# Kernel tuning notes

Hardware: AMD Instinct MI355X
Metric: run time of the kernel (lower is better)

Reference implementation:

```python
import math
import jax, jax.numpy as jnp
import numpy as np

B, S, D, H, DFF, MEM = 4, 1024, 1024, 16, 4096, 256
HD = D // H  # 64
EPS = 1e-5


def _ln(x, g, b):
    mu = jnp.mean(x, axis=-1, keepdims=True)
    var = jnp.mean(jnp.square(x - mu), axis=-1, keepdims=True)
    return (x - mu) * jax.lax.rsqrt(var + EPS) * g + b


def _rope(x, cos, sin):
    # x: (b, h, s, hd); cos/sin: (>=s, hd//2)
    s = x.shape[2]
    xp = x.reshape(*x.shape[:-1], -1, 2)
    x0, x1 = xp[..., 0], xp[..., 1]
    c = cos[:s][None, None]
    sn = sin[:s][None, None]
    r0 = x0 * c - x1 * sn
    r1 = x0 * sn + x1 * c
    return jnp.stack([r0, r1], axis=-1).reshape(x.shape)


def setup_inputs() -> dict:
    key = jax.random.key(0)
    ks = jax.random.split(key, 16)
    p = lambda k, shape: jax.random.normal(k, shape, dtype=jnp.float32) * 0.02

    tgt = jax.random.normal(ks[0], (B, S, D), dtype=jnp.float32)
    memory = jax.random.normal(ks[1], (B, MEM, D), dtype=jnp.float32)

    # causal additive mask (s, s)
    tgt_mask = jnp.where(jnp.tril(jnp.ones((S, S), bool)), 0.0, -1e9).astype(jnp.float32)

    # RoPE freqs, theta=10000
    inv_freq = 1.0 / (10000.0 ** (np.arange(0, HD, 2, dtype=np.float32) / HD))
    ang = np.arange(S, dtype=np.float32)[:, None] * inv_freq[None, :]
    rope_cos = jnp.asarray(np.cos(ang))
    rope_sin = jnp.asarray(np.sin(ang))

    return {
        "tgt": tgt, "memory": memory, "tgt_mask": tgt_mask,
        "rope_cos": rope_cos, "rope_sin": rope_sin,
        "qkv_w": p(ks[2], (3 * D, D)), "qkv_b": jnp.zeros((3 * D,), jnp.float32),
        "out_w": p(ks[3], (D, D)), "out_b": jnp.zeros((D,), jnp.float32),
        "ca_in_w": p(ks[4], (3 * D, D)), "ca_in_b": jnp.zeros((3 * D,), jnp.float32),
        "ca_out_w": p(ks[5], (D, D)), "ca_out_b": jnp.zeros((D,), jnp.float32),
        "ffn_w1": p(ks[6], (DFF, D)), "ffn_b1": jnp.zeros((DFF,), jnp.float32),
        "ffn_w2": p(ks[7], (D, DFF)), "ffn_b2": jnp.zeros((D,), jnp.float32),
        "ln1_g": jnp.ones((D,), jnp.float32), "ln1_b": jnp.zeros((D,), jnp.float32),
        "ln2_g": jnp.ones((D,), jnp.float32), "ln2_b": jnp.zeros((D,), jnp.float32),
        "ln3_g": jnp.ones((D,), jnp.float32), "ln3_b": jnp.zeros((D,), jnp.float32),
    }


def reference(tgt, memory, tgt_mask, rope_cos, rope_sin,
              qkv_w, qkv_b, out_w, out_b,
              ca_in_w, ca_in_b, ca_out_w, ca_out_b,
              ffn_w1, ffn_b1, ffn_w2, ffn_b2,
              ln1_g, ln1_b, ln2_g, ln2_b, ln3_g, ln3_b):
    b, s, d = tgt.shape
    scale = 1.0 / math.sqrt(HD)

    # ---- self-attention with RoPE ----
    x = _ln(tgt, ln1_g, ln1_b)
    qkv = (x @ qkv_w.T + qkv_b).reshape(b, s, 3, H, HD)
    qkv = jnp.transpose(qkv, (2, 0, 3, 1, 4))  # (3, b, h, s, hd)
    q, k, v = qkv[0], qkv[1], qkv[2]
    q = _rope(q, rope_cos, rope_sin)
    k = _rope(k, rope_cos, rope_sin)
    attn = jnp.einsum('bhqd,bhkd->bhqk', q, k) * scale
    attn = attn + tgt_mask[None, None]
    attn = jax.nn.softmax(attn, axis=-1)
    sa = jnp.einsum('bhqk,bhkd->bhqd', attn, v)
    sa = jnp.transpose(sa, (0, 2, 1, 3)).reshape(b, s, d)
    tgt = tgt + (sa @ out_w.T + out_b)

    # ---- cross-attention (standard MHA, no positional encoding) ----
    x = _ln(tgt, ln2_g, ln2_b)
    wq, wk, wv = jnp.split(ca_in_w, 3, axis=0)
    bq, bk, bv = jnp.split(ca_in_b, 3, axis=0)
    m = memory.shape[1]
    cq = (x @ wq.T + bq).reshape(b, s, H, HD).transpose(0, 2, 1, 3)
    ck = (memory @ wk.T + bk).reshape(b, m, H, HD).transpose(0, 2, 1, 3)
    cv = (memory @ wv.T + bv).reshape(b, m, H, HD).transpose(0, 2, 1, 3)
    cattn = jax.nn.softmax(jnp.einsum('bhqd,bhkd->bhqk', cq, ck) * scale, axis=-1)
    co = jnp.einsum('bhqk,bhkd->bhqd', cattn, cv)
    co = jnp.transpose(co, (0, 2, 1, 3)).reshape(b, s, d)
    tgt = tgt + (co @ ca_out_w.T + ca_out_b)

    # ---- FFN (exact GELU, as torch nn.GELU default) ----
    x = _ln(tgt, ln3_g, ln3_b)
    ff = jax.nn.gelu(x @ ffn_w1.T + ffn_b1, approximate=False) @ ffn_w2.T + ffn_b2
    return tgt + ff
```

## Files before the change

kernel.cpp:

```cpp
#include <hip/hip_runtime.h>
#include <hip/hip_bf16.h>


using bf16 = __hip_bfloat16;
typedef __bf16 bf16x8 __attribute__((ext_vector_type(8)));
typedef float f32x4 __attribute__((ext_vector_type(4)));

static constexpr int Bn = 4, Ssz = 1024, Dm = 1024, Hh = 16, HDd = 64, DFFn = 4096, MEMn = 256;

__device__ inline float bf2f(bf16 x) { return __bfloat162float(x); }
__device__ inline bf16 f2bf(float x) { return __float2bfloat16(x); }

__device__ __forceinline__ void gload16(const bf16* g, bf16* l) {
  __builtin_amdgcn_global_load_lds(
      (const __attribute__((address_space(1))) void*)g,
      (__attribute__((address_space(3))) void*)l, 16, 0, 0);
}

__global__ void detect_kernel(const unsigned* __restrict__ cosw, int* __restrict__ flag) {
  if (threadIdx.x == 0) *flag = (cosw[0] == 0x3F800000u) ? 1 : 0;
}

struct CanonArgs {
  const void* src[23];
  void* dst[23];
  int n[23];
};
__global__ __launch_bounds__(256) void canon_all(CanonArgs a, float* __restrict__ resid,
                                                 const int* __restrict__ flagp) {
  const int seg = blockIdx.y;
  const int n4 = a.n[seg] >> 2;
  if (n4 == 0) return;
  const int fl = *flagp;
  if (fl) {
    const float4* s = (const float4*)a.src[seg];
    bf16* d = (bf16*)a.dst[seg];
    for (int i = blockIdx.x * 256 + threadIdx.x; i < n4; i += gridDim.x * 256) {
      float4 v = s[i];
      bf16 t[4] = {f2bf(v.x), f2bf(v.y), f2bf(v.z), f2bf(v.w)};
      *reinterpret_cast<unsigned long long*>(d + i * 4) =
          *reinterpret_cast<unsigned long long*>(t);
      if (seg == 0) *reinterpret_cast<float4*>(resid + i * 4) = v;
    }
  } else {
    const unsigned long long* s = (const unsigned long long*)a.src[seg];
    unsigned long long* d = (unsigned long long*)a.dst[seg];
    for (int i = blockIdx.x * 256 + threadIdx.x; i < n4; i += gridDim.x * 256) {
      unsigned long long v = s[i];
      d[i] = v;
      if (seg == 0) {
        const unsigned short* u = reinterpret_cast<const unsigned short*>(&v);
        float4 f;
        f.x = __uint_as_float(((unsigned)u[0]) << 16);
        f.y = __uint_as_float(((unsigned)u[1]) << 16);
        f.z = __uint_as_float(((unsigned)u[2]) << 16);
        f.w = __uint_as_float(((unsigned)u[3]) << 16);
        *reinterpret_cast<float4*>(resid + i * 4) = f;
      }
    }
  }
}

__global__ __launch_bounds__(256) void ln_kernel(const float* __restrict__ x,
                                                 const bf16* __restrict__ g,
                                                 const bf16* __restrict__ bb,
                                                 bf16* __restrict__ y) {
  const int row = blockIdx.x;
  const float* xr = x + (size_t)row * Dm;
  const int i0 = threadIdx.x * 4;
  float4 v = *reinterpret_cast<const float4*>(xr + i0);
  float s = v.x + v.y + v.z + v.w;
  float ss = v.x * v.x + v.y * v.y + v.z * v.z + v.w * v.w;
#pragma unroll
  for (int o = 32; o > 0; o >>= 1) {
    s += __shfl_down(s, o);
    ss += __shfl_down(ss, o);
  }
  __shared__ float shs[4], shss[4];
  const int wave = threadIdx.x >> 6, lane = threadIdx.x & 63;
  if (lane == 0) { shs[wave] = s; shss[wave] = ss; }
  __syncthreads();
  s = shs[0] + shs[1] + shs[2] + shs[3];
  ss = shss[0] + shss[1] + shss[2] + shss[3];
  const float mu = s * (1.0f / Dm);
  const float var = fmaxf(ss * (1.0f / Dm) - mu * mu, 0.0f);
  const float rs = rsqrtf(var + 1e-5f);
  bf16* yr = y + (size_t)row * Dm + i0;
  float vv[4] = {v.x, v.y, v.z, v.w};
#pragma unroll
  for (int j = 0; j < 4; ++j)
    yr[j] = f2bf((vv[j] - mu) * rs * bf2f(g[i0 + j]) + bf2f(bb[i0 + j]));
}

__global__ __launch_bounds__(256) void gemm_bt(
    const bf16* __restrict__ A, const bf16* __restrict__ W,
    const bf16* __restrict__ bias, bf16* __restrict__ outB, float* __restrict__ outF,
    const float* __restrict__ residIn, float* __restrict__ residOut,
    const int* __restrict__ flagp, int M, int N, int K, int epi) {
  __shared__ bf16 As[64][40];
  __shared__ bf16 Ws[64][40];
  const int tid = threadIdx.x;
  const int m0 = blockIdx.x * 64, n0 = blockIdx.y * 64;
  const int wave = tid >> 6, lane = tid & 63;
  const int wm = wave >> 1, wn = wave & 1;
  const int quad = lane >> 4, m16 = lane & 15;
  const int lr = tid >> 2, lc = (tid & 3) * 8;

  f32x4 acc[2][2] = {};

  const bf16* Ap = A + (size_t)(m0 + lr) * K + lc;
  const bf16* Wp = W + (size_t)(n0 + lr) * K + lc;
  for (int k0 = 0; k0 < K; k0 += 32) {
    float4 av = *reinterpret_cast<const float4*>(Ap + k0);
    float4 wv = *reinterpret_cast<const float4*>(Wp + k0);
    *reinterpret_cast<float4*>(&As[lr][lc]) = av;
    *reinterpret_cast<float4*>(&Ws[lr][lc]) = wv;
    __syncthreads();
    bf16x8 aF[2], bF[2];
#pragma unroll
    for (int t = 0; t < 2; ++t) {
      aF[t] = *reinterpret_cast<const bf16x8*>(&As[wm * 32 + t * 16 + m16][quad * 8]);
      bF[t] = *reinterpret_cast<const bf16x8*>(&Ws[wn * 32 + t * 16 + m16][quad * 8]);
    }
#pragma unroll
    for (int mt = 0; mt < 2; ++mt)
#pragma unroll
      for (int nt = 0; nt < 2; ++nt)
        acc[mt][nt] = __builtin_amdgcn_mfma_f32_16x16x32_bf16(aF[mt], bF[nt], acc[mt][nt], 0, 0, 0);
    __syncthreads();
  }
  const int fl = (epi == 3) ? *flagp : 0;
#pragma unroll
  for (int mt = 0; mt < 2; ++mt) {
#pragma unroll
    for (int nt = 0; nt < 2; ++nt) {
      const int col = n0 + wn * 32 + nt * 16 + m16;
      const float bv = bf2f(bias[col]);
#pragma unroll
      for (int r = 0; r < 4; ++r) {
        const int row = m0 + wm * 32 + mt * 16 + quad * 4 + r;
        const size_t idx = (size_t)row * N + col;
        float v = acc[mt][nt][r] + bv;
        if (epi == 0) {
          outB[idx] = f2bf(v);
        } else if (epi == 1) {
          outB[idx] = f2bf(0.5f * v * (1.0f + erff(v * 0.70710678118654752f)));
        } else if (epi == 2) {
          residOut[idx] = residIn[idx] + v;
        } else {
          const float rr = residIn[idx] + v;
          if (fl) outF[idx] = rr; else outB[idx] = f2bf(rr);
        }
      }
    }
  }
}

__global__ __launch_bounds__(512) void gemm128(
    const bf16* __restrict__ A, const bf16* __restrict__ W,
    const bf16* __restrict__ bias, bf16* __restrict__ outB, float* __restrict__ outF,
    const float* __restrict__ residIn, float* __restrict__ residOut,
    const int* __restrict__ flagp, int M, int N, int K, int epi) {
  __shared__ bf16 As[4][128][32];
  __shared__ bf16 Ws[4][128][32];
  const int tid = threadIdx.x;
  const int wave = tid >> 6, lane = tid & 63;
  const int wm = wave >> 1;
  const int wn = wave & 1;
  const int quad = lane >> 4, m16 = lane & 15;
  const int m0 = blockIdx.x * 128, n0 = blockIdx.y * 128;

  const int sr = tid >> 2;
  const int sc = (tid & 3) * 8;
  const bf16* Ap = A + (size_t)(m0 + sr) * K + sc;
  const bf16* Wp = W + (size_t)(n0 + sr) * K + sc;

  f32x4 acc[2][4] = {};

#define STAGE128(T, BUF)                                   \
  {                                                        \
    const int kk_ = (T) * 32;                              \
    gload16(Ap + kk_, &As[BUF][sr][sc]);                   \
    gload16(Wp + kk_, &Ws[BUF][sr][sc]);                   \
  }

#define READS128(RB)                                                                        \
  _Pragma("unroll") for (int tt = 0; tt < 2; ++tt)                                          \
    aF[tt] = *reinterpret_cast<const bf16x8*>(&As[RB][wm * 32 + tt * 16 + m16][quad * 8]);  \
  _Pragma("unroll") for (int nt = 0; nt < 4; ++nt)                                          \
    bF[nt] = *reinterpret_cast<const bf16x8*>(&Ws[RB][wn * 64 + nt * 16 + m16][quad * 8]);

#define MFMAS128                                                                            \
  _Pragma("unroll") for (int mt = 0; mt < 2; ++mt)                                          \
  _Pragma("unroll") for (int nt = 0; nt < 4; ++nt)                                          \
    acc[mt][nt] = __builtin_amdgcn_mfma_f32_16x16x32_bf16(aF[mt], bF[nt], acc[mt][nt], 0, 0, 0);

  const int nsteps = K >> 5;
  STAGE128(0, 0)
  STAGE128(1, 1)
  STAGE128(2, 2)

  int rb = 0, sb = 3;
  for (int t = 0; t < nsteps - 2; ++t) {
    asm volatile("s_waitcnt vmcnt(4)" ::: "memory");
    __builtin_amdgcn_s_barrier();
    __builtin_amdgcn_sched_barrier(0);
    bf16x8 aF[2], bF[4];
    READS128(rb)
    __builtin_amdgcn_sched_barrier(0);
    if (t + 3 < nsteps) { STAGE128(t + 3, sb) }
    __builtin_amdgcn_sched_barrier(0);
    MFMAS128
    rb = (rb + 1 == 4) ? 0 : rb + 1;
    sb = (sb + 1 == 4) ? 0 : sb + 1;
  }
  {
    asm volatile("s_waitcnt vmcnt(2)" ::: "memory");
    __builtin_amdgcn_s_barrier();
    __builtin_amdgcn_sched_barrier(0);
    bf16x8 aF[2], bF[4];
    READS128(rb)
    MFMAS128
    rb = (rb + 1 == 4) ? 0 : rb + 1;
  }
  {
    asm volatile("s_waitcnt vmcnt(0)" ::: "memory");
    __builtin_amdgcn_s_barrier();
    __builtin_amdgcn_sched_barrier(0);
    bf16x8 aF[2], bF[4];
    READS128(rb)
    MFMAS128
  }
#undef STAGE128
#undef READS128
#undef MFMAS128

  const int fl = (epi == 3) ? *flagp : 0;
#pragma unroll
  for (int mt = 0; mt < 2; ++mt) {
#pragma unroll
    for (int nt = 0; nt < 4; ++nt) {
      const int col = n0 + wn * 64 + nt * 16 + m16;
      const float bv = bf2f(bias[col]);
#pragma unroll
      for (int r = 0; r < 4; ++r) {
        const int row = m0 + wm * 32 + mt * 16 + quad * 4 + r;
        const size_t idx = (size_t)row * N + col;
        float v = acc[mt][nt][r] + bv;
        if (epi == 0) {
          outB[idx] = f2bf(v);
        } else if (epi == 1) {
          outB[idx] = f2bf(0.5f * v * (1.0f + erff(v * 0.70710678118654752f)));
        } else if (epi == 2) {
          residOut[idx] = residIn[idx] + v;
        } else {
          const float rr = residIn[idx] + v;
          if (fl) outF[idx] = rr; else outB[idx] = f2bf(rr);
        }
      }
    }
  }
}

__global__ __launch_bounds__(256) void rope_kernel(bf16* __restrict__ qkv,
                                                   const bf16* __restrict__ cosb,
                                                   const bf16* __restrict__ sinb) {
  const int idx = blockIdx.x * 256 + threadIdx.x;
  const int i = idx & 31;
  const int h = (idx >> 5) & 15;
  const int r = idx >> 9;
  const int s = r & (Ssz - 1);
  const float c = bf2f(cosb[s * 32 + i]);
  const float sn = bf2f(sinb[s * 32 + i]);
  bf16* base = qkv + (size_t)r * (3 * Dm) + h * 64 + 2 * i;
  float x0 = bf2f(base[0]), x1 = bf2f(base[1]);
  base[0] = f2bf(x0 * c - x1 * sn);
  base[1] = f2bf(x0 * sn + x1 * c);
  x0 = bf2f(base[Dm]); x1 = bf2f(base[Dm + 1]);
  base[Dm] = f2bf(x0 * c - x1 * sn);
  base[Dm + 1] = f2bf(x0 * sn + x1 * c);
}

__global__ __launch_bounds__(512) void attn_mfma(
    const bf16* __restrict__ Qb, const bf16* __restrict__ Kb, const bf16* __restrict__ Vb,
    bf16* __restrict__ Ob, int qStride, int kvStride, int kvLen, int causal, float scale) {
  __shared__ bf16 Ks[64][72];
  __shared__ bf16 Vt[64][72];
  __shared__ bf16 Ps[128][72];
  const int tid = threadIdx.x;
  const int wave = tid >> 6, lane = tid & 63;
  const int quad = lane >> 4, m16 = lane & 15;
  const int b = blockIdx.z, h = blockIdx.y;
  const int q0 = blockIdx.x * 128;

  {
    const int sr = tid >> 2, sc = (tid & 3) * 16;
    const bf16* qp = Qb + (size_t)(b * Ssz + q0 + sr) * qStride + h * 64 + sc;
    float4 a = reinterpret_cast<const float4*>(qp)[0];
    float4 bb2 = reinterpret_cast<const float4*>(qp)[1];
    *reinterpret_cast<float4*>(&Ps[sr][sc]) = a;
    *reinterpret_cast<float4*>(&Ps[sr][sc + 8]) = bb2;
  }
  __syncthreads();
  bf16x8 qf[2];
  qf[0] = *reinterpret_cast<const bf16x8*>(&Ps[wave * 16 + m16][quad * 8]);
  qf[1] = *reinterpret_cast<const bf16x8*>(&Ps[wave * 16 + m16][32 + quad * 8]);

  f32x4 oacc[4] = {};
  float mrow[4], lrow[4];
#pragma unroll
  for (int r = 0; r < 4; ++r) { mrow[r] = -30000.0f; lrow[r] = 0.0f; }

  const int wrow0 = q0 + wave * 16;
  const int nk = causal ? (q0 + 128) : kvLen;
  for (int kt = 0; kt < nk; kt += 64) {
    {
      const int dbase = wave * 8;
      const bf16* kp = Kb + (size_t)(b * kvLen + kt + lane) * kvStride + h * 64 + dbase;
      float4 k1 = *reinterpret_cast<const float4*>(kp);
      *reinterpret_cast<float4*>(&Ks[lane][dbase]) = k1;
      const bf16* vp = Vb + (size_t)(b * kvLen + kt + lane) * kvStride + h * 64 + dbase;
      float4 v1 = *reinterpret_cast<const float4*>(vp);
      const bf16* tv = reinterpret_cast<const bf16*>(&v1);
#pragma unroll
      for (int j = 0; j < 8; ++j) Vt[dbase + j][lane] = tv[j];
    }
    __syncthreads();

    const bool live = (causal == 0) || (kt <= wrow0 + 15);
    if (live) {
      f32x4 sacc[4] = {};
#pragma unroll
      for (int nt = 0; nt < 4; ++nt) {
        bf16x8 kf0 = *reinterpret_cast<const bf16x8*>(&Ks[nt * 16 + m16][quad * 8]);
        bf16x8 kf1 = *reinterpret_cast<const bf16x8*>(&Ks[nt * 16 + m16][32 + quad * 8]);
        sacc[nt] = __builtin_amdgcn_mfma_f32_16x16x32_bf16(qf[0], kf0, sacc[nt], 0, 0, 0);
        sacc[nt] = __builtin_amdgcn_mfma_f32_16x16x32_bf16(qf[1], kf1, sacc[nt], 0, 0, 0);
      }
      const bool dmask = (causal != 0) && (kt + 63 > wrow0);
#pragma unroll
      for (int nt = 0; nt < 4; ++nt) {
#pragma unroll
        for (int r = 0; r < 4; ++r) {
          float s = sacc[nt][r] * scale;
          if (dmask && (kt + nt * 16 + m16 > wrow0 + quad * 4 + r)) s = -30000.0f;
          sacc[nt][r] = s;
        }
      }

#pragma unroll
      for (int r = 0; r < 4; ++r) {
        float mx = fmaxf(fmaxf(sacc[0][r], sacc[1][r]), fmaxf(sacc[2][r], sacc[3][r]));
#pragma unroll
        for (int off = 1; off < 16; off <<= 1) mx = fmaxf(mx, __shfl_xor(mx, off));
        const float mn = fmaxf(mrow[r], mx);
        const float corr = __expf(mrow[r] - mn);
        mrow[r] = mn;
        float psum = 0.0f;
#pragma unroll
        for (int nt = 0; nt < 4; ++nt) {
          const float p = __expf(sacc[nt][r] - mn);
          sacc[nt][r] = p;
          psum += p;
        }
#pragma unroll
        for (int off = 1; off < 16; off <<= 1) psum += __shfl_xor(psum, off);
        lrow[r] = lrow[r] * corr + psum;
#pragma unroll
        for (int nt = 0; nt < 4; ++nt) oacc[nt][r] *= corr;
#pragma unroll
        for (int nt = 0; nt < 4; ++nt)
          Ps[wave * 16 + quad * 4 + r][nt * 16 + m16] = f2bf(sacc[nt][r]);
      }
      bf16x8 pf0 = *reinterpret_cast<const bf16x8*>(&Ps[wave * 16 + m16][quad * 8]);
      bf16x8 pf1 = *reinterpret_cast<const bf16x8*>(&Ps[wave * 16 + m16][32 + quad * 8]);
#pragma unroll
      for (int nt = 0; nt < 4; ++nt) {
        bf16x8 vf0 = *reinterpret_cast<const bf16x8*>(&Vt[nt * 16 + m16][quad * 8]);
        bf16x8 vf1 = *reinterpret_cast<const bf16x8*>(&Vt[nt * 16 + m16][32 + quad * 8]);
        oacc[nt] = __builtin_amdgcn_mfma_f32_16x16x32_bf16(pf0, vf0, oacc[nt], 0, 0, 0);
        oacc[nt] = __builtin_amdgcn_mfma_f32_16x16x32_bf16(pf1, vf1, oacc[nt], 0, 0, 0);
      }
    }
    __syncthreads();
  }

  float inv[4];
#pragma unroll
  for (int r = 0; r < 4; ++r) inv[r] = 1.0f / lrow[r];
#pragma unroll
  for (int r = 0; r < 4; ++r) {
    bf16* op = Ob + (size_t)(b * Ssz + q0 + wave * 16 + quad * 4 + r) * Dm + h * 64 + m16;
#pragma unroll
    for (int nt = 0; nt < 4; ++nt) op[nt * 16] = f2bf(oacc[nt][r] * inv[r]);
  }
}

extern "C" void kernel_launch(void* const* d_in, const int* in_sizes, int n_in,
                              void* d_out, int out_size, void* d_ws, size_t ws_size,
                              hipStream_t stream) {
  char* ws = (char*)d_ws;
  int* flagp   = (int*)ws;
  float* resid = (float*)(ws + (1ull << 20));
  bf16* xln    = (bf16*)(ws + (17ull << 20));
  bf16* aout   = (bf16*)(ws + (25ull << 20));
  bf16* big    = (bf16*)(ws + (33ull << 20));
  size_t off   = (65ull << 20);

  detect_kernel<<<1, 64, 0, stream>>>((const unsigned*)d_in[3], flagp);

  CanonArgs ca;
  bf16* c[23];
  for (int i = 0; i < 23; ++i) {
    if (i == 2) { c[i] = nullptr; ca.src[i] = d_in[i]; ca.dst[i] = nullptr; ca.n[i] = 0; continue; }
    c[i] = (bf16*)(ws + off);
    const int n = in_sizes[i];
    off += ((size_t)n * 2 + 255) & ~(size_t)255;
    ca.src[i] = d_in[i];
    ca.dst[i] = c[i];
    ca.n[i] = n;
  }
  canon_all<<<dim3(256, 23), 256, 0, stream>>>(ca, resid, flagp);

  const bf16 *memory = c[1], *rope_cos = c[3], *rope_sin = c[4];
  const bf16 *qkv_w = c[5], *qkv_b = c[6], *out_w = c[7], *out_b = c[8];
  const bf16 *ca_in_w = c[9], *ca_in_b = c[10], *ca_out_w = c[11], *ca_out_b = c[12];
  const bf16 *ffn_w1 = c[13], *ffn_b1 = c[14], *ffn_w2 = c[15], *ffn_b2 = c[16];
  const bf16 *ln1_g = c[17], *ln1_b = c[18], *ln2_g = c[19], *ln2_b = c[20];
  const bf16 *ln3_g = c[21], *ln3_b = c[22];

  bf16* qb = big;
  bf16* kb = (bf16*)(ws + (41ull << 20));
  bf16* vb = (bf16*)(ws + (43ull << 20));
  bf16* outB = (bf16*)d_out;
  float* outF = (float*)d_out;

  const int ROWS = Bn * Ssz;
  const float scale = 0.125f;

  ln_kernel<<<ROWS, 256, 0, stream>>>(resid, ln1_g, ln1_b, xln);
  gemm128<<<dim3(ROWS / 128, (3 * Dm) / 128), 512, 0, stream>>>(
      xln, qkv_w, qkv_b, big, nullptr, nullptr, nullptr, nullptr, ROWS, 3 * Dm, Dm, 0);
  rope_kernel<<<(ROWS * Hh * (HDd / 2)) / 256, 256, 0, stream>>>(big, rope_cos, rope_sin);
  attn_mfma<<<dim3(Ssz / 128, Hh, Bn), 512, 0, stream>>>(
      big, big + Dm, big + 2 * Dm, aout, 3 * Dm, 3 * Dm, Ssz, 1, scale);
  gemm128<<<dim3(ROWS / 128, Dm / 128), 512, 0, stream>>>(
      aout, out_w, out_b, nullptr, nullptr, resid, resid, nullptr, ROWS, Dm, Dm, 2);

  ln_kernel<<<ROWS, 256, 0, stream>>>(resid, ln2_g, ln2_b, xln);
  gemm128<<<dim3(ROWS / 128, Dm / 128), 512, 0, stream>>>(
      xln, ca_in_w, ca_in_b, qb, nullptr, nullptr, nullptr, nullptr, ROWS, Dm, Dm, 0);
  gemm_bt<<<dim3((Bn * MEMn) / 64, Dm / 64), 256, 0, stream>>>(
      memory, ca_in_w + (size_t)Dm * Dm, ca_in_b + Dm, kb, nullptr, nullptr, nullptr, nullptr,
      Bn * MEMn, Dm, Dm, 0);
  gemm_bt<<<dim3((Bn * MEMn) / 64, Dm / 64), 256, 0, stream>>>(
      memory, ca_in_w + (size_t)2 * Dm * Dm, ca_in_b + 2 * Dm, vb, nullptr, nullptr, nullptr, nullptr,
      Bn * MEMn, Dm, Dm, 0);
  attn_mfma<<<dim3(Ssz / 128, Hh, Bn), 512, 0, stream>>>(
      qb, kb, vb, aout, Dm, Dm, MEMn, 0, scale);
  gemm128<<<dim3(ROWS / 128, Dm / 128), 512, 0, stream>>>(
      aout, ca_out_w, ca_out_b, nullptr, nullptr, resid, resid, nullptr, ROWS, Dm, Dm, 2);

  ln_kernel<<<ROWS, 256, 0, stream>>>(resid, ln3_g, ln3_b, xln);
  gemm128<<<dim3(ROWS / 128, DFFn / 128), 512, 0, stream>>>(
      xln, ffn_w1, ffn_b1, big, nullptr, nullptr, nullptr, nullptr, ROWS, DFFn, Dm, 1);
  gemm128<<<dim3(ROWS / 128, Dm / 128), 512, 0, stream>>>(
      big, ffn_w2, ffn_b2, outB, outF, resid, nullptr, flagp, ROWS, Dm, DFFn, 3);
}
```

Baseline: 519.6 us.

## Add 256x256-tile GEMM kernel for QKV and FFN1 projections

Introduces a gemm256 kernel using 256x256 output tiles with double-buffered LDS staging via global_load_lds and swizzled reads, with each wave computing a 128x64 sub-tile. It replaces the 128x128 GEMM for the QKV projection and the first FFN layer to raise arithmetic intensity and cut global loads per FLOP. The larger tile needs 128KB LDS and 128 accumulator registers per thread, which limits occupancy. It also yields fewer blocks: 16x12=192 for QKV and 16x16=256 for FFN1, which may underfill the 256 CUs.

Result: no change. 519.4 us (-0.0%).

```diff
diff --git a/kernel.cpp b/kernel.cpp
--- a/kernel.cpp
+++ b/kernel.cpp
@@ -262,6 +262,84 @@
   }
 }
 
+__global__ __launch_bounds__(512) void gemm256(
+    const bf16* __restrict__ A, const bf16* __restrict__ W,
+    const bf16* __restrict__ bias, bf16* __restrict__ outB,
+    int M, int N, int K, int epi) {
+  __shared__ bf16 Abuf[2][256 * 64];
+  __shared__ bf16 Bbuf[2][256 * 64];
+  const int tid = threadIdx.x;
+  const int wave = tid >> 6, lane = tid & 63;
+  const int wm = wave >> 2, wn = wave & 3;
+  const int quad = lane >> 4, m16 = lane & 15;
+  const int m0 = blockIdx.x * 256, n0 = blockIdx.y * 256;
+  const int lr8 = lane >> 3, lc8 = lane & 7;
+  const int gch = (lc8 ^ lr8) * 8;
+  const int swz = m16 & 7;
+
+  f32x4 acc[8][4] = {};
+
+#define STAGE256(T, BUF)                                                         \
+  { const int kb_ = (T) * 64 + gch;                                              \
+    _Pragma("unroll") for (int i = 0; i < 4; ++i) {                              \
+      const int rr = (wave * 4 + i) * 8 + lr8;                                   \
+      gload16(A + (size_t)(m0 + rr) * K + kb_, &Abuf[BUF][rr * 64 + lc8 * 8]);   \
+      gload16(W + (size_t)(n0 + rr) * K + kb_, &Bbuf[BUF][rr * 64 + lc8 * 8]);   \
+    } }
+
+  const int nsteps = K >> 6;
+  STAGE256(0, 0)
+  for (int t = 0; t < nsteps; ++t) {
+    asm volatile("s_waitcnt vmcnt(0)" ::: "memory");
+    __builtin_amdgcn_s_barrier();
+    __builtin_amdgcn_sched_barrier(0);
+    const int rb = t & 1;
+    bf16x8 aF[2][8], bF[2][4];
+#pragma unroll
+    for (int kk = 0; kk < 2; ++kk) {
+      const int cswz = ((quad + 4 * kk) ^ swz) * 8;
+#pragma unroll
+      for (int tt = 0; tt < 8; ++tt)
+        aF[kk][tt] = *reinterpret_cast<const bf16x8*>(
+            &Abuf[rb][(wm * 128 + tt * 16 + m16) * 64 + cswz]);
+#pragma unroll
+      for (int nt = 0; nt < 4; ++nt)
+        bF[kk][nt] = *reinterpret_cast<const bf16x8*>(
+            &Bbuf[rb][(wn * 64 + nt * 16 + m16) * 64 + cswz]);
+    }
+    __builtin_amdgcn_sched_barrier(0);
+    if (t + 1 < nsteps) { STAGE256(t + 1, rb ^ 1) }
+    __builtin_amdgcn_sched_barrier(0);
+#pragma unroll
+    for (int kk = 0; kk < 2; ++kk)
+#pragma unroll
+      for (int mt = 0; mt < 8; ++mt)
+#pragma unroll
+        for (int nt = 0; nt < 4; ++nt)
+          acc[mt][nt] = __builtin_amdgcn_mfma_f32_16x16x32_bf16(
+              aF[kk][mt], bF[kk][nt], acc[mt][nt], 0, 0, 0);
+  }
+#undef STAGE256
+
+#pragma unroll
+  for (int mt = 0; mt < 8; ++mt) {
+#pragma unroll
+    for (int nt = 0; nt < 4; ++nt) {
+      const int col = n0 + wn * 64 + nt * 16 + m16;
+      const float bv = bf2f(bias[col]);
+#pragma unroll
+      for (int r = 0; r < 4; ++r) {
+        const int row = m0 + wm * 128 + mt * 16 + quad * 4 + r;
+        const size_t idx = (size_t)row * N + col;
+        float v = acc[mt][nt][r] + bv;
+        outB[idx] = (epi == 1)
+                        ? f2bf(0.5f * v * (1.0f + erff(v * 0.70710678118654752f)))
+                        : f2bf(v);
+      }
+    }
+  }
+}
+
 __global__ __launch_bounds__(256) void rope_kernel(bf16* __restrict__ qkv,
                                                    const bf16* __restrict__ cosb,
                                                    const bf16* __restrict__ sinb) {
@@ -439,8 +517,8 @@
   const float scale = 0.125f;
 
   ln_kernel<<<ROWS, 256, 0, stream>>>(resid, ln1_g, ln1_b, xln);
-  gemm128<<<dim3(ROWS / 128, (3 * Dm) / 128), 512, 0, stream>>>(
-      xln, qkv_w, qkv_b, big, nullptr, nullptr, nullptr, nullptr, ROWS, 3 * Dm, Dm, 0);
+  gemm256<<<dim3(ROWS / 256, (3 * Dm) / 256), 512, 0, stream>>>(
+      xln, qkv_w, qkv_b, big, ROWS, 3 * Dm, Dm, 0);
   rope_kernel<<<(ROWS * Hh * (HDd / 2)) / 256, 256, 0, stream>>>(big, rope_cos, rope_sin);
   attn_mfma<<<dim3(Ssz / 128, Hh, Bn), 512, 0, stream>>>(
       big, big + Dm, big + 2 * Dm, aout, 3 * Dm, 3 * Dm, Ssz, 1, scale);
@@ -462,8 +540,8 @@
       aout, ca_out_w, ca_out_b, nullptr, nullptr, resid, resid, nullptr, ROWS, Dm, Dm, 2);
 
   ln_kernel<<<ROWS, 256, 0, stream>>>(resid, ln3_g, ln3_b, xln);
-  gemm128<<<dim3(ROWS / 128, DFFn / 128), 512, 0, stream>>>(
-      xln, ffn_w1, ffn_b1, big, nullptr, nullptr, nullptr, nullptr, ROWS, DFFn, Dm, 1);
+  gemm256<<<dim3(ROWS / 256, DFFn / 256), 512, 0, stream>>>(
+      xln, ffn_w1, ffn_b1, big, ROWS, DFFn, Dm, 1);
   gemm128<<<dim3(ROWS / 128, Dm / 128), 512, 0, stream>>>(
       big, ffn_w2, ffn_b2, outB, outF, resid, nullptr, flagp, ROWS, Dm, DFFn, 3);
 }
```
